# Optimization experiments

Measured on AMD Instinct MI355X. Metric: run time of the kernel, lower is better.

The kernel has to match this reference:

```python
import jax, jax.numpy as jnp
import numpy as np
import math

B, L, D, H, MAX_K = 8, 4096, 2048, 16, 1024
HD = D // H


def setup_inputs() -> dict:
    key = jax.random.key(0)
    ks = jax.random.split(key, 20)
    x = jax.random.normal(ks[0], (B, L, D), dtype=jnp.float32)
    register = jax.random.normal(ks[1], (B, D), dtype=jnp.float32)
    # mask with exactly MAX_K True per row -> max_k == MAX_K, no ragged padding
    perms = jax.vmap(lambda k: jax.random.permutation(k, L))(jax.random.split(ks[2], B))
    sel = perms[:, :MAX_K]
    mask = jnp.zeros((B, L), dtype=bool).at[jnp.arange(B)[:, None], sel].set(True)
    s = 1.0 / math.sqrt(D)
    def lin(k):
        k1, k2 = jax.random.split(k)
        return (jax.random.uniform(k1, (D, D), jnp.float32, -s, s),
                jax.random.uniform(k2, (D,), jnp.float32, -s, s))
    Wq, bq = lin(ks[3]); Wk, bk = lin(ks[4]); Wv, bv = lin(ks[5])
    Wrk, brk = lin(ks[6]); Wrv, brv = lin(ks[7]); Wo, bo = lin(ks[8])
    return {"x": x, "mask": mask, "register": register,
            "Wq": Wq, "bq": bq, "Wk": Wk, "bk": bk, "Wv": Wv, "bv": bv,
            "Wrk": Wrk, "brk": brk, "Wrv": Wrv, "brv": brv, "Wo": Wo, "bo": bo}


def reference(x, mask, register, Wq, bq, Wk, bk, Wv, bv, Wrk, brk, Wrv, brv, Wo, bo):
    Bb, Ll, Dd = x.shape
    scale = math.sqrt(HD)
    # stable argsort puts True(=selected) tokens first, in ascending position order
    idx = jnp.argsort(jnp.logical_not(mask), axis=1, stable=True)[:, :MAX_K]  # [B,K]
    pos = idx
    sig = jnp.take_along_axis(x, idx[:, :, None], axis=1)  # [B,K,D]
    Q = (sig @ Wq.T + bq).reshape(Bb, MAX_K, H, HD)
    Kt = (sig @ Wk.T + bk)
    Vt = (sig @ Wv.T + bv)
    Kr = (register @ Wrk.T + brk)[:, None, :]  # [B,1,D]
    Vr = (register @ Wrv.T + brv)[:, None, :]
    Kall = jnp.concatenate([Kt, Kr], axis=1).reshape(Bb, MAX_K + 1, H, HD)
    Vall = jnp.concatenate([Vt, Vr], axis=1).reshape(Bb, MAX_K + 1, H, HD)
    scores = jnp.einsum('bqhd,bkhd->bhqk', Q, Kall) / scale  # [B,H,K,K+1]
    causal = jnp.where(pos[:, :, None] < pos[:, None, :], -1e9, 0.0)  # [B,K,K]
    full_mask = jnp.concatenate([causal, jnp.zeros((Bb, MAX_K, 1), x.dtype)], axis=2)[:, None]
    attn = jax.nn.softmax(scores + full_mask, axis=-1)
    out = jnp.einsum('bhqk,bkhd->bqhd', attn, Vall).reshape(Bb, MAX_K, Dd)
    y = out @ Wo.T + bo
    res = x.at[jnp.arange(Bb)[:, None], idx].set(y)
    return res
```

## Files before the change

### kernel.cpp

```cpp
#include <hip/hip_runtime.h>
#include <hip/hip_bf16.h>

#define B_  8
#define L_  4096
#define D_  2048
#define H_  16
#define HD_ 128
#define MK_ 1024
#define VTP 1040

typedef __attribute__((ext_vector_type(8))) short short8;
typedef __attribute__((ext_vector_type(4))) float f32x4;

__device__ inline unsigned short f2bf(float f) {
  unsigned int u = __float_as_uint(f);
  unsigned int r = (u + 0x7fffu + ((u >> 16) & 1u)) >> 16;
  return (unsigned short)r;
}

__device__ __forceinline__ void gload_lds16(const void* g, void* l) {
  __builtin_amdgcn_global_load_lds(
      (const __attribute__((address_space(1))) void*)g,
      (__attribute__((address_space(3))) void*)l, 16, 0, 0);
}

__global__ void detect_mask_kernel(const unsigned char* __restrict__ mask, int* flag) {
  __shared__ int cnt;
  if (threadIdx.x == 0) cnt = 0;
  __syncthreads();
  int local = 0;
  for (int i = threadIdx.x; i < B_ * L_; i += 256) local += (mask[i] != 0);
  atomicAdd(&cnt, local);
  __syncthreads();
  if (threadIdx.x == 0) {
    int t = 0;
    if (cnt == B_ * MK_)      t = 0;
    else if (cnt == 2 * MK_)  t = 1;
    else if (cnt == 4 * MK_)  t = 2;
    *flag = t;
  }
}

__global__ void build_rowmap_kernel(const void* __restrict__ maskv,
                                    const int* __restrict__ flag,
                                    int* __restrict__ rowmap) {
  int b = blockIdx.x;
  int tid = threadIdx.x;
  int t = *flag;
  __shared__ int cnts[256];
  unsigned char loc[16];
  int c = 0;
  for (int j = 0; j < 16; ++j) {
    int pos = tid * 16 + j;
    int mv;
    if (t == 1)      mv = ((const int*)maskv)[b * L_ + pos] != 0;
    else if (t == 2) mv = ((const float*)maskv)[b * L_ + pos] != 0.0f;
    else             mv = ((const unsigned char*)maskv)[b * L_ + pos] != 0;
    loc[j] = (unsigned char)mv; c += mv;
  }
  cnts[tid] = c;
  __syncthreads();
  for (int off = 1; off < 256; off <<= 1) {
    int v = (tid >= off) ? cnts[tid - off] : 0;
    __syncthreads();
    cnts[tid] += v;
    __syncthreads();
  }
  int rank = cnts[tid] - c;
  for (int j = 0; j < 16; ++j) {
    if (loc[j]) {
      if (rank < MK_) rowmap[b * MK_ + rank] = b * L_ + tid * 16 + j;
      ++rank;
    }
  }
}

__global__ __launch_bounds__(256) void gather_sig_kernel(const float* __restrict__ x,
                                                         const int* __restrict__ rowmap,
                                                         unsigned short* __restrict__ sig) {
  int row = blockIdx.x;
  const float* src = x + (size_t)rowmap[row] * D_;
  unsigned short* dst = sig + (size_t)row * D_;
  int tid = threadIdx.x;
  float4 a = ((const float4*)src)[tid * 2];
  float4 b4 = ((const float4*)src)[tid * 2 + 1];
  uint4 o;
  o.x = f2bf(a.x)  | ((unsigned)f2bf(a.y)  << 16);
  o.y = f2bf(a.z)  | ((unsigned)f2bf(a.w)  << 16);
  o.z = f2bf(b4.x) | ((unsigned)f2bf(b4.y) << 16);
  o.w = f2bf(b4.z) | ((unsigned)f2bf(b4.w) << 16);
  *(uint4*)(dst + tid * 8) = o;
}

__global__ __launch_bounds__(256) void conv_bf16_kernel(const float* __restrict__ W0,
                                                        const float* __restrict__ W1,
                                                        const float* __restrict__ W2,
                                                        const float* __restrict__ W3,
                                                        unsigned short* __restrict__ Wb) {
  const size_t per = (size_t)D_ * D_;
  int slab = blockIdx.x >> 11;
  const float* W = (slab == 0) ? W0 : (slab == 1) ? W1 : (slab == 2) ? W2 : W3;
  size_t i = ((size_t)(blockIdx.x & 2047) * 256 + threadIdx.x) * 8;
  float4 a = *(const float4*)(W + i);
  float4 b4 = *(const float4*)(W + i + 4);
  uint4 o;
  o.x = f2bf(a.x)  | ((unsigned)f2bf(a.y)  << 16);
  o.y = f2bf(a.z)  | ((unsigned)f2bf(a.w)  << 16);
  o.z = f2bf(b4.x) | ((unsigned)f2bf(b4.y) << 16);
  o.w = f2bf(b4.z) | ((unsigned)f2bf(b4.w) << 16);
  *(uint4*)(Wb + slab * per + i) = o;
}

__global__ __launch_bounds__(256) void reg_kv_kernel(
    const float* __restrict__ reg, const float* __restrict__ Wrk, const float* __restrict__ brk,
    const float* __restrict__ Wrv, const float* __restrict__ brv,
    unsigned short* __restrict__ Kb, unsigned short* __restrict__ Vt) {
  int gw = (blockIdx.x * 256 + threadIdx.x) >> 6;
  int lane = threadIdx.x & 63;
  int mat = gw >> 11;
  int n = gw & 2047;
  const float* W = mat ? Wrv : Wrk;
  const float* wrow = W + (size_t)n * D_;
  float s[8] = {};
  for (int j = 0; j < 8; ++j) {
    int e = j * 256 + lane * 4;
    float4 wv = *(const float4*)(wrow + e);
#pragma unroll
    for (int b = 0; b < 8; ++b) {
      float4 rv = *(const float4*)(reg + (size_t)b * D_ + e);
      s[b] += wv.x * rv.x + wv.y * rv.y + wv.z * rv.z + wv.w * rv.w;
    }
  }
#pragma unroll
  for (int off = 32; off; off >>= 1)
#pragma unroll
    for (int b = 0; b < 8; ++b) s[b] += __shfl_down(s[b], off);
  if (lane == 0) {
    float bias = (mat ? brv : brk)[n];
#pragma unroll
    for (int b = 0; b < 8; ++b) {
      unsigned short v = f2bf(s[b] + bias);
      if (mat) {
        Vt[(((size_t)b * 16 + (n >> 7)) * 128 + (n & 127)) * VTP + 1024] = v;
      } else {
        Kb[((size_t)b * 1025 + 1024) * D_ + n] = v;
      }
    }
  }
}

template<int FUSED>
__global__ __launch_bounds__(512, 2) void gemm8_kernel(
    const unsigned short* __restrict__ A, const unsigned short* __restrict__ Bw,
    const float* __restrict__ b0, const float* __restrict__ b1, const float* __restrict__ b2,
    void* __restrict__ O0, void* __restrict__ O1, void* __restrict__ O2,
    const int* __restrict__ rowmap, float qalpha, int nbt, int matfix) {
  __shared__ __align__(16) unsigned short lds[4][2][8192];
  int tid = threadIdx.x, lane = tid & 63, w = tid >> 6;
  int g = lane >> 4, l15 = lane & 15;
  int wm = w >> 2, wn = w & 3;

  int bid = blockIdx.x;
  int xcd = bid & 7, j = bid >> 3;
  int mb = xcd * 4 + j / nbt, nb = j % nbt;
  int m0 = mb * 256, n0 = nb * 256;

  f32x4 acc[2][4][4] = {};

#define STAGE(kt, c) {                                                          \
    const unsigned short* src0 = (c) ? Bw : A;                                  \
    int base0 = (c) ? n0 : m0;                                                  \
    int sg = (lane & 3) ^ ((lane >> 3) & 3);                                    \
    _Pragma("unroll")                                                           \
    for (int i_ = 0; i_ < 2; ++i_) {                                            \
      int row = (w * 2 + i_) * 16 + (lane >> 2);                                \
      gload_lds16(src0 + (size_t)(base0 + row) * D_ + (kt) * 32 + sg * 8,       \
                  &lds[(kt) & 3][c][(w * 2 + i_) * 512]);                       \
    }                                                                           \
  }

  STAGE(0, 0); STAGE(0, 1);
  STAGE(1, 0); STAGE(1, 1);
  STAGE(2, 0); STAGE(2, 1);
  asm volatile("s_waitcnt vmcnt(8)" ::: "memory");
  __builtin_amdgcn_s_barrier();

  int sw8 = (g ^ ((l15 >> 1) & 3)) * 8;

  short8 afE[4], afO[4], bfA[4], bfB[4];
  {
    const unsigned short* Ab = &lds[0][0][0];
    const unsigned short* Bb = &lds[0][1][0];
#pragma unroll
    for (int nf = 0; nf < 4; ++nf)
      bfA[nf] = *(const short8*)(Bb + (wn * 64 + nf * 16 + l15) * 32 + sw8);
#pragma unroll
    for (int mf = 0; mf < 4; ++mf)
      afE[mf] = *(const short8*)(Ab + (wm * 128 + mf * 16 + l15) * 32 + sw8);
  }

#define KTILE(kt, bfC, bfN)                                                       \
  {                                                                               \
    const unsigned short* Abuf = &lds[(kt) & 3][0][0];                            \
    _Pragma("unroll")                                                             \
    for (int mf = 0; mf < 4; ++mf)                                                \
      afO[mf] = *(const short8*)(Abuf + (wm * 128 + 64 + mf * 16 + l15) * 32 + sw8); \
    if ((kt) + 3 < 64) STAGE((kt) + 3, 0);                                        \
    asm volatile("s_waitcnt lgkmcnt(4)" ::: "memory");                            \
    __builtin_amdgcn_sched_barrier(0);                                            \
    __builtin_amdgcn_s_setprio(1);                                                \
    _Pragma("unroll")                                                             \
    for (int mf = 0; mf < 4; ++mf)                                                \
      _Pragma("unroll")                                                           \
      for (int nf = 0; nf < 4; ++nf)                                              \
        acc[0][mf][nf] = __builtin_amdgcn_mfma_f32_16x16x32_bf16(afE[mf], bfC[nf], acc[0][mf][nf], 0, 0, 0); \
    __builtin_amdgcn_s_setprio(0);                                                \
    if ((kt) <= 60)      asm volatile("s_waitcnt vmcnt(6)" ::: "memory");         \
    else if ((kt) == 61) asm volatile("s_waitcnt vmcnt(4)" ::: "memory");         \
    else if ((kt) == 62) asm volatile("s_waitcnt vmcnt(0)" ::: "memory");         \
    if ((kt) < 63) {                                                              \
      __builtin_amdgcn_s_barrier();                                               \
      const unsigned short* An = &lds[((kt) + 1) & 3][0][0];                      \
      const unsigned short* Bn = &lds[((kt) + 1) & 3][1][0];                      \
      _Pragma("unroll")                                                           \
      for (int nf = 0; nf < 4; ++nf)                                              \
        bfN[nf] = *(const short8*)(Bn + (wn * 64 + nf * 16 + l15) * 32 + sw8);    \
      _Pragma("unroll")                                                           \
      for (int mf = 0; mf < 4; ++mf)                                              \
        afE[mf] = *(const short8*)(An + (wm * 128 + mf * 16 + l15) * 32 + sw8);   \
      if ((kt) + 3 < 64) STAGE((kt) + 3, 1);                                      \
      asm volatile("s_waitcnt lgkmcnt(8)" ::: "memory");                          \
    } else {                                                                      \
      asm volatile("s_waitcnt lgkmcnt(0)" ::: "memory");                          \
    }                                                                             \
    __builtin_amdgcn_sched_barrier(0);                                            \
    __builtin_amdgcn_s_setprio(1);                                                \
    _Pragma("unroll")                                                             \
    for (int mf = 0; mf < 4; ++mf)                                                \
      _Pragma("unroll")                                                           \
      for (int nf = 0; nf < 4; ++nf)                                              \
        acc[1][mf][nf] = __builtin_amdgcn_mfma_f32_16x16x32_bf16(afO[mf], bfC[nf], acc[1][mf][nf], 0, 0, 0); \
    __builtin_amdgcn_s_setprio(0);                                                \
    if ((kt) < 63) __builtin_amdgcn_s_barrier();                                  \
  }

  for (int kt2 = 0; kt2 < 32; ++kt2) {
    KTILE(2 * kt2,     bfA, bfB);
    KTILE(2 * kt2 + 1, bfB, bfA);
  }
#undef KTILE
#undef STAGE

  int mat = 0;
  const float* bias = b0;
  float alpha = 1.0f;
  int n0l = n0;
  if (FUSED) {
    mat = (matfix >= 0) ? matfix : (n0 >> 11);
    bias = (mat == 0) ? b0 : ((mat == 1) ? b1 : b2);
    alpha = (mat == 0) ? qalpha : 1.0f;
    n0l = n0 & 2047;
  }

#pragma unroll
  for (int ph = 0; ph < 2; ++ph) {
#pragma unroll
    for (int mf = 0; mf < 4; ++mf) {
#pragma unroll
      for (int nf = 0; nf < 4; ++nf) {
        int nn = n0l + wn * 64 + nf * 16 + l15;
        float bvv = bias[nn];
        int m = m0 + wm * 128 + ph * 64 + mf * 16 + g * 4;
        if (FUSED) {
          if (mat == 2) {
            int bb = m >> 10, tok = m & 1023;
            size_t base = (((size_t)bb * 16 + (nn >> 7)) * 128 + (nn & 127)) * VTP + tok;
            uint2 u;
            u.x = f2bf(acc[ph][mf][nf][0] + bvv) | ((unsigned)f2bf(acc[ph][mf][nf][1] + bvv) << 16);
            u.y = f2bf(acc[ph][mf][nf][2] + bvv) | ((unsigned)f2bf(acc[ph][mf][nf][3] + bvv) << 16);
            *(uint2*)((unsigned short*)O2 + base) = u;
          } else {
            unsigned short* out = (mat == 0) ? (unsigned short*)O0 : (unsigned short*)O1;
#pragma unroll
            for (int r = 0; r < 4; ++r) {
              float v = (acc[ph][mf][nf][r] + bvv) * alpha;
              int mm = m + r;
              int row = (mat == 1) ? mm + (mm >> 10) : mm;
              out[(size_t)row * D_ + nn] = f2bf(v);
            }
          }
        } else {
#pragma unroll
          for (int r = 0; r < 4; ++r) {
            int row = rowmap[m + r];
            ((float*)O0)[(size_t)row * D_ + nn] = acc[ph][mf][nf][r] + bvv;
          }
        }
      }
    }
  }
}

__device__ __forceinline__ void stage_k(const unsigned short* Kbase, unsigned short* dst,
                                        int kv0, int w, int lane) {
#pragma unroll
  for (int i = 0; i < 2; ++i) {
    int ib = w * 2 + i;
    int row = ib * 4 + (lane >> 4);
    int sl = (lane & 15) ^ (row & 7);
    int krow = kv0 + row; if (krow > MK_) krow = MK_;
    gload_lds16(Kbase + (size_t)krow * D_ + sl * 8, dst + ib * 512);
  }
}
__device__ __forceinline__ void stage_v(const unsigned short* Vbase, unsigned short* dst,
                                        int kv0, int w, int lane) {
#pragma unroll
  for (int i = 0; i < 2; ++i) {
    int ib = w * 2 + i;
    int row = ib * 8 + (lane >> 3);
    int sl = (lane & 7) ^ (row & 7);
    gload_lds16(Vbase + (size_t)row * VTP + kv0 + sl * 8, dst + ib * 512);
  }
}

#define NF4 16777216

__global__ __launch_bounds__(512) void attn_kernel(
    const unsigned short* __restrict__ Qb, const unsigned short* __restrict__ Kb,
    const unsigned short* __restrict__ Vt, unsigned short* __restrict__ Ob,
    const float4* __restrict__ xsrc, float4* __restrict__ xdst) {
  int bx = blockIdx.x;
  int gq = bx >> 7;
  int qi = 7 - gq;
  int bh = bx & 127;
  int b = bh >> 4, h = bh & 15;
  int tid = threadIdx.x, lane = tid & 63, w = tid >> 6;
  int g = lane >> 4, l15 = lane & 15;
  int q0 = qi * 128;
  int nt = 2 * qi + 3;

  size_t cpyBase = ((size_t)128 * (18 * gq - gq * gq) + (size_t)(bx & 127) * nt) * 2048;

  __shared__ __align__(16) unsigned short Ks[64 * 128];
  __shared__ __align__(16) unsigned short Vts[128 * 64];
  __shared__ __align__(16) unsigned short Ps[8][16][72];

  const unsigned short* Kbase = Kb + (size_t)b * 1025 * D_ + h * HD_;
  const unsigned short* Vbase = Vt + (size_t)bh * 128 * VTP;

  short8 qf[4];
  {
    const unsigned short* qrow = Qb + (size_t)(b * MK_ + q0 + w * 16 + l15) * D_ + h * HD_;
#pragma unroll
    for (int kk = 0; kk < 4; ++kk) qf[kk] = *(const short8*)(qrow + kk * 32 + g * 8);
  }

  f32x4 oacc[8] = {};
  float mrow[4], lrow[4];
#pragma unroll
  for (int r = 0; r < 4; ++r) { mrow[r] = -__builtin_inff(); lrow[r] = 0.f; }

  int qminw = q0 + w * 16;

  stage_k(Kbase, Ks, 0, w, lane);

  for (int t = 0; t < nt; ++t) {
    int kv0 = (t < nt - 1) ? t * 64 : MK_;

    size_t ci[4];
    float4 cv[4];
    {
      size_t i0 = cpyBase + (size_t)t * 2048 + tid;
#pragma unroll
      for (int jj = 0; jj < 4; ++jj) {
        size_t ix = i0 + jj * 512;
        ci[jj] = ix < NF4 ? ix : (NF4 - 1);
        cv[jj] = xsrc[ci[jj]];
      }
    }

    stage_v(Vbase, Vts, kv0, w, lane);
    if (t == 0) asm volatile("s_waitcnt vmcnt(6)" ::: "memory");
    else        asm volatile("s_waitcnt vmcnt(10)" ::: "memory");
    __builtin_amdgcn_s_barrier();

    bool active = (t == nt - 1) || (t * 64 <= qminw + 15);
    f32x4 sacc[4] = {};
    if (active) {
      __builtin_amdgcn_s_setprio(1);
#pragma unroll
      for (int kk = 0; kk < 4; ++kk) {
#pragma unroll
        for (int nf = 0; nf < 4; ++nf) {
          int krow = nf * 16 + l15;
          int sw = (kk * 4 + g) ^ (krow & 7);
          short8 kf = *(const short8*)(Ks + krow * 128 + sw * 8);
          sacc[nf] = __builtin_amdgcn_mfma_f32_16x16x32_bf16(qf[kk], kf, sacc[nf], 0, 0, 0);
        }
      }
      __builtin_amdgcn_s_setprio(0);
    }

    __builtin_amdgcn_s_barrier();
    if (t + 1 < nt) {
      int kv1 = (t + 1 < nt - 1) ? (t + 1) * 64 : MK_;
      stage_k(Kbase, Ks, kv1, w, lane);
    }

    if (active) {
      if (t == nt - 1) {
#pragma unroll
        for (int nf = 0; nf < 4; ++nf) {
          int col = nf * 16 + l15;
          if (col != 0) {
#pragma unroll
            for (int r = 0; r < 4; ++r) sacc[nf][r] = -1e9f;
          }
        }
      } else if (t * 64 + 63 > qminw) {
        int qb = qminw - t * 64 + g * 4;
#pragma unroll
        for (int nf = 0; nf < 4; ++nf) {
          int col = nf * 16 + l15;
#pragma unroll
          for (int r = 0; r < 4; ++r)
            if (col > qb + r) sacc[nf][r] = -1e9f;
        }
      }

      float pm[4]; bool need = false;
#pragma unroll
      for (int r = 0; r < 4; ++r) {
        float mx = fmaxf(fmaxf(sacc[0][r], sacc[1][r]), fmaxf(sacc[2][r], sacc[3][r]));
        mx = fmaxf(mx, __shfl_xor(mx, 1));
        mx = fmaxf(mx, __shfl_xor(mx, 2));
        mx = fmaxf(mx, __shfl_xor(mx, 4));
        mx = fmaxf(mx, __shfl_xor(mx, 8));
        pm[r] = mx;
        need |= (mx > mrow[r] + 8.0f);
      }
      if (__any((int)need)) {
#pragma unroll
        for (int r = 0; r < 4; ++r) {
          float mnew = fmaxf(mrow[r], pm[r]);
          float sf = exp2f(mrow[r] - mnew);
          mrow[r] = mnew;
          lrow[r] *= sf;
#pragma unroll
          for (int i = 0; i < 8; ++i) oacc[i][r] *= sf;
        }
      }
      float rs[4] = {0.f, 0.f, 0.f, 0.f};
#pragma unroll
      for (int nf = 0; nf < 4; ++nf) {
#pragma unroll
        for (int r = 0; r < 4; ++r) {
          float p = exp2f(sacc[nf][r] - mrow[r]);
          sacc[nf][r] = p;
          rs[r] += p;
        }
      }
#pragma unroll
      for (int r = 0; r < 4; ++r) {
        float s = rs[r];
        s += __shfl_xor(s, 1);
        s += __shfl_xor(s, 2);
        s += __shfl_xor(s, 4);
        s += __shfl_xor(s, 8);
        lrow[r] += s;
      }
#pragma unroll
      for (int nf = 0; nf < 4; ++nf)
#pragma unroll
        for (int r = 0; r < 4; ++r)
          Ps[w][g * 4 + r][nf * 16 + l15] = f2bf(sacc[nf][r]);
    }

    if (t + 1 < nt) asm volatile("s_waitcnt vmcnt(2)" ::: "memory");
    else            asm volatile("s_waitcnt vmcnt(0)" ::: "memory");

#pragma unroll
    for (int jj = 0; jj < 4; ++jj) xdst[ci[jj]] = cv[jj];

    __builtin_amdgcn_s_barrier();

    if (active) {
      __builtin_amdgcn_s_setprio(1);
#pragma unroll
      for (int kk = 0; kk < 2; ++kk) {
        short8 pf = *(const short8*)(&Ps[w][l15][kk * 32 + g * 8]);
#pragma unroll
        for (int nf = 0; nf < 8; ++nf) {
          int vrow = nf * 16 + l15;
          int sw = (kk * 4 + g) ^ (vrow & 7);
          short8 vf = *(const short8*)(Vts + vrow * 64 + sw * 8);
          oacc[nf] = __builtin_amdgcn_mfma_f32_16x16x32_bf16(pf, vf, oacc[nf], 0, 0, 0);
        }
      }
      __builtin_amdgcn_s_setprio(0);
    }
    __builtin_amdgcn_s_barrier();
  }

#pragma unroll
  for (int nf = 0; nf < 8; ++nf) {
#pragma unroll
    for (int r = 0; r < 4; ++r) {
      size_t row = (size_t)b * MK_ + q0 + w * 16 + g * 4 + r;
      Ob[row * D_ + h * HD_ + nf * 16 + l15] = f2bf(oacc[nf][r] / lrow[r]);
    }
  }
}

extern "C" void kernel_launch(void* const* d_in, const int* in_sizes, int n_in,
                              void* d_out, int out_size, void* d_ws, size_t ws_size,
                              hipStream_t stream) {
  const float* x    = (const float*)d_in[0];
  const void*  mask = d_in[1];
  const float* reg  = (const float*)d_in[2];
  const float* Wq   = (const float*)d_in[3];
  const float* bq   = (const float*)d_in[4];
  const float* Wk   = (const float*)d_in[5];
  const float* bk   = (const float*)d_in[6];
  const float* Wv   = (const float*)d_in[7];
  const float* bv   = (const float*)d_in[8];
  const float* Wrk  = (const float*)d_in[9];
  const float* brk  = (const float*)d_in[10];
  const float* Wrv  = (const float*)d_in[11];
  const float* brv  = (const float*)d_in[12];
  const float* Wo   = (const float*)d_in[13];
  const float* bo   = (const float*)d_in[14];

  char* ws = (char*)d_ws;
  int* flag            = (int*)ws;
  int* rowmap          = (int*)(ws + 256);
  char* p = ws + 66048;
  unsigned short* sig = (unsigned short*)p;              p += (size_t)8192 * 2048 * 2;
  unsigned short* Qb  = (unsigned short*)p;              p += (size_t)8192 * 2048 * 2;
  unsigned short* Kb  = (unsigned short*)p;              p += (size_t)8200 * 2048 * 2;
  unsigned short* Vtb = (unsigned short*)p;              p += ((size_t)16384 * VTP + 64) * 2;
  unsigned short* Wbf = (unsigned short*)p;
  unsigned short* Ob  = sig;

  const size_t need_fused = (size_t)(p - ws) + (size_t)8192 * 2048 * 2;
  const bool fused = (ws_size >= need_fused);

  detect_mask_kernel<<<1, 256, 0, stream>>>((const unsigned char*)mask, flag);
  build_rowmap_kernel<<<8, 256, 0, stream>>>(mask, flag, rowmap);
  gather_sig_kernel<<<8192, 256, 0, stream>>>(x, rowmap, sig);
  reg_kv_kernel<<<1024, 256, 0, stream>>>(reg, Wrk, brk, Wrv, brv, Kb, Vtb);

  const float qalpha = 0.08838834764831845f * 1.4426950408889634f;
  const size_t per = (size_t)2048 * 2048;

  if (fused) {
    conv_bf16_kernel<<<8192, 256, 0, stream>>>(Wq, Wk, Wv, Wo, Wbf);
    gemm8_kernel<1><<<768, 512, 0, stream>>>(sig, Wbf, bq, bk, bv, Qb, Kb, Vtb,
                                             nullptr, qalpha, 24, -1);
    attn_kernel<<<1024, 512, 0, stream>>>(Qb, Kb, Vtb, Ob, (const float4*)x, (float4*)d_out);
    gemm8_kernel<0><<<256, 512, 0, stream>>>(Ob, Wbf + 3 * per, bo, nullptr, nullptr,
                                             d_out, nullptr, nullptr, rowmap, 1.0f, 8, -1);
  } else {
    conv_bf16_kernel<<<2048, 256, 0, stream>>>(Wq, Wq, Wq, Wq, Wbf);
    gemm8_kernel<1><<<256, 512, 0, stream>>>(sig, Wbf, bq, bk, bv, Qb, Kb, Vtb,
                                             nullptr, qalpha, 8, 0);
    conv_bf16_kernel<<<2048, 256, 0, stream>>>(Wk, Wk, Wk, Wk, Wbf);
    gemm8_kernel<1><<<256, 512, 0, stream>>>(sig, Wbf, bq, bk, bv, Qb, Kb, Vtb,
                                             nullptr, qalpha, 8, 1);
    conv_bf16_kernel<<<2048, 256, 0, stream>>>(Wv, Wv, Wv, Wv, Wbf);
    gemm8_kernel<1><<<256, 512, 0, stream>>>(sig, Wbf, bq, bk, bv, Qb, Kb, Vtb,
                                             nullptr, qalpha, 8, 2);
    attn_kernel<<<1024, 512, 0, stream>>>(Qb, Kb, Vtb, Ob, (const float4*)x, (float4*)d_out);
    conv_bf16_kernel<<<2048, 256, 0, stream>>>(Wo, Wo, Wo, Wo, Wbf);
    gemm8_kernel<0><<<256, 512, 0, stream>>>(Ob, Wbf, bo, nullptr, nullptr,
                                             d_out, nullptr, nullptr, rowmap, 1.0f, 8, -1);
  }
}
```

Baseline: 532.5 us.

## Restructure GEMM main loop to K=64 tiles with double buffering

Rewrites the bf16 GEMM main loop so each stage loads a 64-wide K slice into one of two LDS buffers, replacing the previous four-deep ring of 32-wide slices. It uses an XOR swizzle over 8 slots and runs 32 iterations instead of 64, which halves the barrier count per K. The trade-off is shallower prefetch: each tile waits on vmcnt(0) before its barrier, so global load latency is hidden by only one tile of MFMA work.

```diff
diff --git a/kernel.cpp b/kernel.cpp
--- a/kernel.cpp
+++ b/kernel.cpp
@@ -155,7 +155,7 @@
     const float* __restrict__ b0, const float* __restrict__ b1, const float* __restrict__ b2,
     void* __restrict__ O0, void* __restrict__ O1, void* __restrict__ O2,
     const int* __restrict__ rowmap, float qalpha, int nbt, int matfix) {
-  __shared__ __align__(16) unsigned short lds[4][2][8192];
+  __shared__ __align__(16) unsigned short lds[2][2][16384];
   int tid = threadIdx.x, lane = tid & 63, w = tid >> 6;
   int g = lane >> 4, l15 = lane & 15;
   int wm = w >> 2, wn = w & 3;
@@ -167,89 +167,100 @@
 
   f32x4 acc[2][4][4] = {};
 
-#define STAGE(kt, c) {                                                          \
-    const unsigned short* src0 = (c) ? Bw : A;                                  \
-    int base0 = (c) ? n0 : m0;                                                  \
-    int sg = (lane & 3) ^ ((lane >> 3) & 3);                                    \
-    _Pragma("unroll")                                                           \
-    for (int i_ = 0; i_ < 2; ++i_) {                                            \
-      int row = (w * 2 + i_) * 16 + (lane >> 2);                                \
-      gload_lds16(src0 + (size_t)(base0 + row) * D_ + (kt) * 32 + sg * 8,       \
-                  &lds[(kt) & 3][c][(w * 2 + i_) * 512]);                       \
-    }                                                                           \
-  }
-
-  STAGE(0, 0); STAGE(0, 1);
-  STAGE(1, 0); STAGE(1, 1);
-  STAGE(2, 0); STAGE(2, 1);
-  asm volatile("s_waitcnt vmcnt(8)" ::: "memory");
+  size_t aoff[4], boff[4];
+  int ldsoff[4];
+#pragma unroll
+  for (int i = 0; i < 4; ++i) {
+    int chunk = tid + i * 512;
+    int row = chunk >> 3;
+    int gslot = (chunk & 7) ^ (row & 7);
+    aoff[i] = (size_t)(m0 + row) * D_ + gslot * 8;
+    boff[i] = (size_t)(n0 + row) * D_ + gslot * 8;
+    ldsoff[i] = (w * 64 + i * 512) * 8;
+  }
+
+#define STAGE_A(kt, BUF) {                                              \
+    _Pragma("unroll")                                                   \
+    for (int i_ = 0; i_ < 4; ++i_)                                      \
+      gload_lds16(A + aoff[i_] + (kt) * 64, &lds[BUF][0][ldsoff[i_]]);  \
+  }
+#define STAGE_B(kt, BUF) {                                              \
+    _Pragma("unroll")                                                   \
+    for (int i_ = 0; i_ < 4; ++i_)                                      \
+      gload_lds16(Bw + boff[i_] + (kt) * 64, &lds[BUF][1][ldsoff[i_]]); \
+  }
+#define RD_A(dst, BUF, h, kk) {                                         \
+    _Pragma("unroll")                                                   \
+    for (int mf_ = 0; mf_ < 4; ++mf_) {                                 \
+      int r_ = wm * 128 + (h) * 64 + mf_ * 16 + l15;                    \
+      dst[mf_] = *(const short8*)(&lds[BUF][0][r_ * 64 + (((kk) * 4 + g) ^ (r_ & 7)) * 8]); } \
+  }
+#define RD_B(dst, BUF, kk) {                                            \
+    _Pragma("unroll")                                                   \
+    for (int nf_ = 0; nf_ < 4; ++nf_) {                                 \
+      int r_ = wn * 64 + nf_ * 16 + l15;                                \
+      dst[nf_] = *(const short8*)(&lds[BUF][1][r_ * 64 + (((kk) * 4 + g) ^ (r_ & 7)) * 8]); } \
+  }
+#define MFMA16(h, af, bf) {                                             \
+    _Pragma("unroll")                                                   \
+    for (int mf_ = 0; mf_ < 4; ++mf_)                                   \
+      _Pragma("unroll")                                                 \
+      for (int nf_ = 0; nf_ < 4; ++nf_)                                 \
+        acc[h][mf_][nf_] = __builtin_amdgcn_mfma_f32_16x16x32_bf16(af[mf_], bf[nf_], acc[h][mf_][nf_], 0, 0, 0); \
+  }
+
+  STAGE_A(0, 0); STAGE_B(0, 0);
+  asm volatile("s_waitcnt vmcnt(0)" ::: "memory");
   __builtin_amdgcn_s_barrier();
 
-  int sw8 = (g ^ ((l15 >> 1) & 3)) * 8;
-
-  short8 afE[4], afO[4], bfA[4], bfB[4];
-  {
-    const unsigned short* Ab = &lds[0][0][0];
-    const unsigned short* Bb = &lds[0][1][0];
-#pragma unroll
-    for (int nf = 0; nf < 4; ++nf)
-      bfA[nf] = *(const short8*)(Bb + (wn * 64 + nf * 16 + l15) * 32 + sw8);
-#pragma unroll
-    for (int mf = 0; mf < 4; ++mf)
-      afE[mf] = *(const short8*)(Ab + (wm * 128 + mf * 16 + l15) * 32 + sw8);
-  }
-
-#define KTILE(kt, bfC, bfN)                                                       \
-  {                                                                               \
-    const unsigned short* Abuf = &lds[(kt) & 3][0][0];                            \
-    _Pragma("unroll")                                                             \
-    for (int mf = 0; mf < 4; ++mf)                                                \
-      afO[mf] = *(const short8*)(Abuf + (wm * 128 + 64 + mf * 16 + l15) * 32 + sw8); \
-    if ((kt) + 3 < 64) STAGE((kt) + 3, 0);                                        \
-    asm volatile("s_waitcnt lgkmcnt(4)" ::: "memory");                            \
-    __builtin_amdgcn_sched_barrier(0);                                            \
-    __builtin_amdgcn_s_setprio(1);                                                \
-    _Pragma("unroll")                                                             \
-    for (int mf = 0; mf < 4; ++mf)                                                \
-      _Pragma("unroll")                                                           \
-      for (int nf = 0; nf < 4; ++nf)                                              \
-        acc[0][mf][nf] = __builtin_amdgcn_mfma_f32_16x16x32_bf16(afE[mf], bfC[nf], acc[0][mf][nf], 0, 0, 0); \
-    __builtin_amdgcn_s_setprio(0);                                                \
-    if ((kt) <= 60)      asm volatile("s_waitcnt vmcnt(6)" ::: "memory");         \
-    else if ((kt) == 61) asm volatile("s_waitcnt vmcnt(4)" ::: "memory");         \
-    else if ((kt) == 62) asm volatile("s_waitcnt vmcnt(0)" ::: "memory");         \
-    if ((kt) < 63) {                                                              \
-      __builtin_amdgcn_s_barrier();                                               \
-      const unsigned short* An = &lds[((kt) + 1) & 3][0][0];                      \
-      const unsigned short* Bn = &lds[((kt) + 1) & 3][1][0];                      \
-      _Pragma("unroll")                                                           \
-      for (int nf = 0; nf < 4; ++nf)                                              \
-        bfN[nf] = *(const short8*)(Bn + (wn * 64 + nf * 16 + l15) * 32 + sw8);    \
-      _Pragma("unroll")                                                           \
-      for (int mf = 0; mf < 4; ++mf)                                              \
-        afE[mf] = *(const short8*)(An + (wm * 128 + mf * 16 + l15) * 32 + sw8);   \
-      if ((kt) + 3 < 64) STAGE((kt) + 3, 1);                                      \
-      asm volatile("s_waitcnt lgkmcnt(8)" ::: "memory");                          \
-    } else {                                                                      \
-      asm volatile("s_waitcnt lgkmcnt(0)" ::: "memory");                          \
-    }                                                                             \
-    __builtin_amdgcn_sched_barrier(0);                                            \
-    __builtin_amdgcn_s_setprio(1);                                                \
-    _Pragma("unroll")                                                             \
-    for (int mf = 0; mf < 4; ++mf)                                                \
-      _Pragma("unroll")                                                           \
-      for (int nf = 0; nf < 4; ++nf)                                              \
-        acc[1][mf][nf] = __builtin_amdgcn_mfma_f32_16x16x32_bf16(afO[mf], bfC[nf], acc[1][mf][nf], 0, 0, 0); \
-    __builtin_amdgcn_s_setprio(0);                                                \
-    if ((kt) < 63) __builtin_amdgcn_s_barrier();                                  \
-  }
-
-  for (int kt2 = 0; kt2 < 32; ++kt2) {
-    KTILE(2 * kt2,     bfA, bfB);
-    KTILE(2 * kt2 + 1, bfB, bfA);
+  short8 afE[4], afO[4], bf0[4], bf1[4];
+
+#define KTILE(kt, BUF)                                                    \
+  {                                                                       \
+    RD_B(bf0, BUF, 0); RD_B(bf1, BUF, 1); RD_A(afE, BUF, 0, 0);           \
+                                                       \
+    RD_A(afO, BUF, 0, 1);                                                 \
+    if ((kt) + 1 < 32) STAGE_A((kt) + 1, BUF ^ 1);                        \
+    asm volatile("s_waitcnt lgkmcnt(4)" ::: "memory");                    \
+    __builtin_amdgcn_sched_barrier(0);                                    \
+    __builtin_amdgcn_s_setprio(1);                                        \
+    MFMA16(0, afE, bf0);                                                  \
+    __builtin_amdgcn_s_setprio(0);                                        \
+                                                       \
+    RD_A(afE, BUF, 1, 0);                                                 \
+    if ((kt) + 1 < 32) STAGE_B((kt) + 1, BUF ^ 1);                        \
+    asm volatile("s_waitcnt lgkmcnt(4)" ::: "memory");                    \
+    __builtin_amdgcn_sched_barrier(0);                                    \
+    __builtin_amdgcn_s_setprio(1);                                        \
+    MFMA16(0, afO, bf1);                                                  \
+    __builtin_amdgcn_s_setprio(0);                                        \
+                                                       \
+    RD_A(afO, BUF, 1, 1);                                                 \
+    asm volatile("s_waitcnt lgkmcnt(4)" ::: "memory");                    \
+    __builtin_amdgcn_sched_barrier(0);                                    \
+    __builtin_amdgcn_s_setprio(1);                                        \
+    MFMA16(1, afE, bf0);                                                  \
+    __builtin_amdgcn_s_setprio(0);                                        \
+                                                       \
+    asm volatile("s_waitcnt lgkmcnt(0)" ::: "memory");                    \
+    __builtin_amdgcn_sched_barrier(0);                                    \
+    __builtin_amdgcn_s_setprio(1);                                        \
+    MFMA16(1, afO, bf1);                                                  \
+    __builtin_amdgcn_s_setprio(0);                                        \
+    asm volatile("s_waitcnt vmcnt(0)" ::: "memory");                      \
+    __builtin_amdgcn_s_barrier();                                         \
+  }
+
+  for (int kt2 = 0; kt2 < 16; ++kt2) {
+    KTILE(2 * kt2,     0);
+    KTILE(2 * kt2 + 1, 1);
   }
 #undef KTILE
-#undef STAGE
+#undef MFMA16
+#undef RD_A
+#undef RD_B
+#undef STAGE_A
+#undef STAGE_B
 
   int mat = 0;
   const float* bias = b0;
```

After: 532.0 us. About the same (-0.1%).
